# Performance work log

Hardware: AMD Instinct MI355X
Metric: run time of the kernel (lower is better)

The kernel has to match this reference:

```python
import jax, jax.numpy as jnp
import numpy as np

N = 262144
DIM = 256
H = 4
HD = DIM // H
B = 8192


def setup_inputs() -> dict:
    key = jax.random.key(0)
    ks = jax.random.split(key, 7)
    x = jax.random.normal(ks[0], (N, DIM), dtype=jnp.float32)
    batch = jnp.sort(jax.random.randint(ks[1], (N,), 0, B))
    batch = batch.at[-1].set(B - 1)  # ensure max(batch)+1 == B
    query = jax.random.normal(ks[2], (H, HD), dtype=jnp.float32)
    key_w = jax.random.normal(ks[3], (DIM, DIM), dtype=jnp.float32) * (DIM ** -0.5)
    key_b = jax.random.normal(ks[4], (DIM,), dtype=jnp.float32) * 0.02
    value_w = jax.random.normal(ks[5], (DIM, DIM), dtype=jnp.float32) * (DIM ** -0.5)
    value_b = jax.random.normal(ks[6], (DIM,), dtype=jnp.float32) * 0.02
    return {"x": x, "batch": batch, "query": query, "key_w": key_w,
            "key_b": key_b, "value_w": value_w, "value_b": value_b}


def reference(x, batch, query, key_w, key_b, value_w, value_b):
    scale = HD ** -0.5
    n = x.shape[0]
    k = (x @ key_w.T + key_b).reshape(n, H, HD)
    v = (x @ value_w.T + value_b).reshape(n, H, HD)
    attn = jnp.einsum('nhd,hd->nh', k, query) * scale  # [N,H]
    attn = jnp.clip(attn, -20.0, 20.0)
    # Faithful to source: scatter reduce='max' is buggy and returns zeros,
    # so attn_max == 0 and attn_shifted == attn (clamp makes exp safe).
    attn_exp = jnp.exp(attn)
    attn_sum = jax.ops.segment_sum(attn_exp, batch, num_segments=B)  # [B,H]
    attn_norm = attn_exp / (attn_sum[batch] + 1e-8)  # [N,H]
    weighted = attn_norm[:, :, None] * v  # [N,H,HD]
    pooled = jax.ops.segment_sum(weighted, batch, num_segments=B)  # [B,H,HD]
    return pooled.reshape(B, -1)
```

## Files before the change

kernel.cpp:

```cpp
#include <hip/hip_runtime.h>
#include <hip/hip_bf16.h>

#define NROWS 262144
#define DIM   256
#define NH    4
#define HD    64
#define NSEG  8192

#define WS_QK 65536
#define WS_QB 66560

__global__ __launch_bounds__(256) void prep_kernel(
    const float* __restrict__ query,
    const float* __restrict__ key_w,
    const float* __restrict__ key_b,
    const float* __restrict__ value_w,
    float* __restrict__ ws) {
  float* vwT = ws;
  float* qk  = ws + WS_QK;
  float* qb  = ws + WS_QB;
  const int t = threadIdx.x;

  if (blockIdx.x < 64) {
    __shared__ float tile[32][33];
    const int bx = (blockIdx.x & 7) * 32;
    const int by = (blockIdx.x >> 3) * 32;
    const int tx = t & 31, ty = t >> 5;
#pragma unroll
    for (int k = 0; k < 4; ++k)
      tile[ty + 8 * k][tx] = value_w[(by + ty + 8 * k) * DIM + bx + tx];
    __syncthreads();
#pragma unroll
    for (int k = 0; k < 4; ++k)
      vwT[(bx + ty + 8 * k) * DIM + by + tx] = tile[tx][ty + 8 * k];
  } else {
    const float scale = 0.125f;
#pragma unroll
    for (int h = 0; h < NH; ++h) {
      float acc = 0.f;
      for (int d = 0; d < HD; ++d)
        acc += query[h * HD + d] * key_w[(h * HD + d) * DIM + t];
      qk[h * DIM + t] = acc * scale;
    }
    if (t < NH) {
      float acc = 0.f;
      for (int d = 0; d < HD; ++d)
        acc += query[t * HD + d] * key_b[t * HD + d];
      qb[t] = acc * scale;
    }
  }
}

__global__ __launch_bounds__(256) void main_kernel(
    const float* __restrict__ x,
    const int* __restrict__ batch,
    const float* __restrict__ value_b,
    const float* __restrict__ ws,
    float* __restrict__ out) {
  const float* vwT = ws;
  const float* qk  = ws + WS_QK;
  const float* qb  = ws + WS_QB;

  __shared__ float zu[4][NH][DIM];
  __shared__ float sSh[4][NH];

  const int t = threadIdx.x;
  const int w = t >> 6;
  const int l = t & 63;
  const int b = blockIdx.x * 4 + w;

  int lo = 0, hi = NROWS;
  while (lo < hi) { int mid = (lo + hi) >> 1; if (batch[mid] < b) lo = mid + 1; else hi = mid; }
  const int start = lo;
  hi = NROWS;
  while (lo < hi) { int mid = (lo + hi) >> 1; if (batch[mid] < b + 1) lo = mid + 1; else hi = mid; }
  const int end = lo;

  const float4 q0 = *(const float4*)(qk + 0 * DIM + 4 * l);
  const float4 q1 = *(const float4*)(qk + 1 * DIM + 4 * l);
  const float4 q2 = *(const float4*)(qk + 2 * DIM + 4 * l);
  const float4 q3 = *(const float4*)(qk + 3 * DIM + 4 * l);
  const float qb0 = qb[0], qb1 = qb[1], qb2 = qb[2], qb3 = qb[3];

  float4 z0 = {0.f, 0.f, 0.f, 0.f}, z1 = z0, z2 = z0, z3 = z0;
  float s0 = 0.f, s1 = 0.f, s2 = 0.f, s3 = 0.f;

  for (int n = start; n < end; ++n) {
    const float4 xv = *(const float4*)(x + (size_t)n * DIM + 4 * l);
    float p0 = q0.x * xv.x + q0.y * xv.y + q0.z * xv.z + q0.w * xv.w;
    float p1 = q1.x * xv.x + q1.y * xv.y + q1.z * xv.z + q1.w * xv.w;
    float p2 = q2.x * xv.x + q2.y * xv.y + q2.z * xv.z + q2.w * xv.w;
    float p3 = q3.x * xv.x + q3.y * xv.y + q3.z * xv.z + q3.w * xv.w;
#pragma unroll
    for (int m = 1; m < 64; m <<= 1) {
      p0 += __shfl_xor(p0, m, 64);
      p1 += __shfl_xor(p1, m, 64);
      p2 += __shfl_xor(p2, m, 64);
      p3 += __shfl_xor(p3, m, 64);
    }
    const float e0 = __expf(fminf(fmaxf(p0 + qb0, -20.f), 20.f));
    const float e1 = __expf(fminf(fmaxf(p1 + qb1, -20.f), 20.f));
    const float e2 = __expf(fminf(fmaxf(p2 + qb2, -20.f), 20.f));
    const float e3 = __expf(fminf(fmaxf(p3 + qb3, -20.f), 20.f));
    s0 += e0; s1 += e1; s2 += e2; s3 += e3;
    z0.x += e0 * xv.x; z0.y += e0 * xv.y; z0.z += e0 * xv.z; z0.w += e0 * xv.w;
    z1.x += e1 * xv.x; z1.y += e1 * xv.y; z1.z += e1 * xv.z; z1.w += e1 * xv.w;
    z2.x += e2 * xv.x; z2.y += e2 * xv.y; z2.z += e2 * xv.z; z2.w += e2 * xv.w;
    z3.x += e3 * xv.x; z3.y += e3 * xv.y; z3.z += e3 * xv.z; z3.w += e3 * xv.w;
  }

  *(float4*)&zu[w][0][4 * l] = z0;
  *(float4*)&zu[w][1][4 * l] = z1;
  *(float4*)&zu[w][2][4 * l] = z2;
  *(float4*)&zu[w][3][4 * l] = z3;
  if (l == 0) { sSh[w][0] = s0; sSh[w][1] = s1; sSh[w][2] = s2; sSh[w][3] = s3; }
  __syncthreads();

  const int h = t >> 6;
  float inv[4], cb[4];
#pragma unroll
  for (int seg = 0; seg < 4; ++seg) {
    const float sv = sSh[seg][h];
    const float iv = 1.f / (sv + 1e-8f);
    inv[seg] = iv;
    cb[seg]  = sv * iv;
  }
  float a0 = 0.f, a1 = 0.f, a2 = 0.f, a3 = 0.f;
  for (int i = 0; i < DIM; i += 4) {
    const float w0 = vwT[(i + 0) * DIM + t];
    const float w1 = vwT[(i + 1) * DIM + t];
    const float w2 = vwT[(i + 2) * DIM + t];
    const float w3 = vwT[(i + 3) * DIM + t];
    const float4 za = *(const float4*)&zu[0][h][i];
    const float4 zb = *(const float4*)&zu[1][h][i];
    const float4 zc = *(const float4*)&zu[2][h][i];
    const float4 zd = *(const float4*)&zu[3][h][i];
    a0 += w0 * za.x + w1 * za.y + w2 * za.z + w3 * za.w;
    a1 += w0 * zb.x + w1 * zb.y + w2 * zb.z + w3 * zb.w;
    a2 += w0 * zc.x + w1 * zc.y + w2 * zc.z + w3 * zc.w;
    a3 += w0 * zd.x + w1 * zd.y + w2 * zd.z + w3 * zd.w;
  }
  const float vb = value_b[t];
  const int b0 = blockIdx.x * 4;
  out[(size_t)(b0 + 0) * DIM + t] = a0 * inv[0] + cb[0] * vb;
  out[(size_t)(b0 + 1) * DIM + t] = a1 * inv[1] + cb[1] * vb;
  out[(size_t)(b0 + 2) * DIM + t] = a2 * inv[2] + cb[2] * vb;
  out[(size_t)(b0 + 3) * DIM + t] = a3 * inv[3] + cb[3] * vb;
}

extern "C" void kernel_launch(void* const* d_in, const int* in_sizes, int n_in,
                              void* d_out, int out_size, void* d_ws, size_t ws_size,
                              hipStream_t stream) {
  const float* x       = (const float*)d_in[0];
  const int*   batch   = (const int*)d_in[1];
  const float* query   = (const float*)d_in[2];
  const float* key_w   = (const float*)d_in[3];
  const float* key_b   = (const float*)d_in[4];
  const float* value_w = (const float*)d_in[5];
  const float* value_b = (const float*)d_in[6];
  float* out = (float*)d_out;
  float* ws  = (float*)d_ws;

  prep_kernel<<<65, 256, 0, stream>>>(query, key_w, key_b, value_w, ws);
  main_kernel<<<2048, 256, 0, stream>>>(x, batch, value_b, ws, out);
}
```

Before: 456.1 us.

## Process eight segments per block with 4-row unroll and cheaper head reductions

Each block now handles eight segments, two per wave, so every vwT weight load in the projection epilogue is reused across twice as many segments. Segment bounds come from one cooperative binary search into shared memory. The per-row dot product uses a transpose-style partial reduction, so each lane ends up owning one head's score, cutting shuffles from 24 to 6 per row. The row loop is unrolled by four to give more loads in flight. The prep kernel also spreads the qk computation over four blocks. In exchange there are half as many blocks, with more shared memory and registers per block, which may lower occupancy and latency hiding.

```diff
diff --git a/kernel.cpp b/kernel.cpp
--- a/kernel.cpp
+++ b/kernel.cpp
@@ -6,9 +6,11 @@
 #define NH    4
 #define HD    64
 #define NSEG  8192
+#define SPB   8
+#define NBLK  (NSEG / SPB)
 
 #define WS_QK 65536
-#define WS_QB 66560
+#define WS_QB (WS_QK + NH * DIM)
 
 __global__ __launch_bounds__(256) void prep_kernel(
     const float* __restrict__ query,
@@ -33,22 +35,36 @@
 #pragma unroll
     for (int k = 0; k < 4; ++k)
       vwT[(bx + ty + 8 * k) * DIM + by + tx] = tile[tx][ty + 8 * k];
+  } else if (blockIdx.x < 68) {
+    const int h = blockIdx.x - 64;
+    float acc = 0.f;
+#pragma unroll 8
+    for (int d = 0; d < HD; ++d)
+      acc += query[h * HD + d] * key_w[(h * HD + d) * DIM + t];
+    qk[h * DIM + t] = acc * 0.125f;
   } else {
-    const float scale = 0.125f;
-#pragma unroll
-    for (int h = 0; h < NH; ++h) {
-      float acc = 0.f;
-      for (int d = 0; d < HD; ++d)
-        acc += query[h * HD + d] * key_w[(h * HD + d) * DIM + t];
-      qk[h * DIM + t] = acc * scale;
-    }
     if (t < NH) {
       float acc = 0.f;
       for (int d = 0; d < HD; ++d)
         acc += query[t * HD + d] * key_b[t * HD + d];
-      qb[t] = acc * scale;
-    }
-  }
+      qb[t] = acc * 0.125f;
+    }
+  }
+}
+
+__device__ __forceinline__ float head_partial(float p0, float p1, float p2,
+                                              float p3, int l) {
+  const bool odd = (l & 1) != 0;
+  float sa = odd ? p0 : p1;
+  float ra = __shfl_xor(sa, 1, 64);
+  float vl = (odd ? p1 : p0) + ra;
+  float sb = odd ? p2 : p3;
+  float rb = __shfl_xor(sb, 1, 64);
+  float vh = (odd ? p3 : p2) + rb;
+  const bool g2 = (l & 2) != 0;
+  float sc = g2 ? vl : vh;
+  float rc = __shfl_xor(sc, 2, 64);
+  return (g2 ? vh : vl) + rc;
 }
 
 __global__ __launch_bounds__(256) void main_kernel(
@@ -61,91 +77,163 @@
   const float* qk  = ws + WS_QK;
   const float* qb  = ws + WS_QB;
 
-  __shared__ float zu[4][NH][DIM];
-  __shared__ float sSh[4][NH];
+  __shared__ float zu[SPB][NH][DIM];
+  __shared__ float sSh[SPB][NH];
+  __shared__ int   segb[SPB + 1];
 
   const int t = threadIdx.x;
   const int w = t >> 6;
   const int l = t & 63;
-  const int b = blockIdx.x * 4 + w;
-
-  int lo = 0, hi = NROWS;
-  while (lo < hi) { int mid = (lo + hi) >> 1; if (batch[mid] < b) lo = mid + 1; else hi = mid; }
-  const int start = lo;
-  hi = NROWS;
-  while (lo < hi) { int mid = (lo + hi) >> 1; if (batch[mid] < b + 1) lo = mid + 1; else hi = mid; }
-  const int end = lo;
-
+
+  if (t <= SPB) {
+    const int target = blockIdx.x * SPB + t;
+    int lo = 0, hi = NROWS;
+    while (lo < hi) { int mid = (lo + hi) >> 1; if (batch[mid] < target) lo = mid + 1; else hi = mid; }
+    segb[t] = lo;
+  }
+  __syncthreads();
+
+  const int h4 = l & 3;
   const float4 q0 = *(const float4*)(qk + 0 * DIM + 4 * l);
   const float4 q1 = *(const float4*)(qk + 1 * DIM + 4 * l);
   const float4 q2 = *(const float4*)(qk + 2 * DIM + 4 * l);
   const float4 q3 = *(const float4*)(qk + 3 * DIM + 4 * l);
-  const float qb0 = qb[0], qb1 = qb[1], qb2 = qb[2], qb3 = qb[3];
-
-  float4 z0 = {0.f, 0.f, 0.f, 0.f}, z1 = z0, z2 = z0, z3 = z0;
-  float s0 = 0.f, s1 = 0.f, s2 = 0.f, s3 = 0.f;
-
-  for (int n = start; n < end; ++n) {
-    const float4 xv = *(const float4*)(x + (size_t)n * DIM + 4 * l);
-    float p0 = q0.x * xv.x + q0.y * xv.y + q0.z * xv.z + q0.w * xv.w;
-    float p1 = q1.x * xv.x + q1.y * xv.y + q1.z * xv.z + q1.w * xv.w;
-    float p2 = q2.x * xv.x + q2.y * xv.y + q2.z * xv.z + q2.w * xv.w;
-    float p3 = q3.x * xv.x + q3.y * xv.y + q3.z * xv.z + q3.w * xv.w;
-#pragma unroll
-    for (int m = 1; m < 64; m <<= 1) {
-      p0 += __shfl_xor(p0, m, 64);
-      p1 += __shfl_xor(p1, m, 64);
-      p2 += __shfl_xor(p2, m, 64);
-      p3 += __shfl_xor(p3, m, 64);
-    }
-    const float e0 = __expf(fminf(fmaxf(p0 + qb0, -20.f), 20.f));
-    const float e1 = __expf(fminf(fmaxf(p1 + qb1, -20.f), 20.f));
-    const float e2 = __expf(fminf(fmaxf(p2 + qb2, -20.f), 20.f));
-    const float e3 = __expf(fminf(fmaxf(p3 + qb3, -20.f), 20.f));
-    s0 += e0; s1 += e1; s2 += e2; s3 += e3;
-    z0.x += e0 * xv.x; z0.y += e0 * xv.y; z0.z += e0 * xv.z; z0.w += e0 * xv.w;
-    z1.x += e1 * xv.x; z1.y += e1 * xv.y; z1.z += e1 * xv.z; z1.w += e1 * xv.w;
-    z2.x += e2 * xv.x; z2.y += e2 * xv.y; z2.z += e2 * xv.z; z2.w += e2 * xv.w;
-    z3.x += e3 * xv.x; z3.y += e3 * xv.y; z3.z += e3 * xv.z; z3.w += e3 * xv.w;
-  }
-
-  *(float4*)&zu[w][0][4 * l] = z0;
-  *(float4*)&zu[w][1][4 * l] = z1;
-  *(float4*)&zu[w][2][4 * l] = z2;
-  *(float4*)&zu[w][3][4 * l] = z3;
-  if (l == 0) { sSh[w][0] = s0; sSh[w][1] = s1; sSh[w][2] = s2; sSh[w][3] = s3; }
+  const float qbv = qb[h4];
+
+#pragma unroll
+  for (int ss = 0; ss < 2; ++ss) {
+    const int seg = 2 * w + ss;
+    const int start = segb[seg], end = segb[seg + 1];
+    float4 z0 = {0.f, 0.f, 0.f, 0.f}, z1 = z0, z2 = z0, z3 = z0;
+    float s0 = 0.f, s1 = 0.f, s2 = 0.f, s3 = 0.f;
+    const float* xp = x + (size_t)start * DIM + 4 * l;
+    int n = start;
+
+    for (; n + 4 <= end; n += 4, xp += 4 * DIM) {
+      const float4 xv0 = *(const float4*)(xp);
+      const float4 xv1 = *(const float4*)(xp + DIM);
+      const float4 xv2 = *(const float4*)(xp + 2 * DIM);
+      const float4 xv3 = *(const float4*)(xp + 3 * DIM);
+      float v0, v1, v2, v3;
+      {
+        float p0 = q0.x * xv0.x + q0.y * xv0.y + q0.z * xv0.z + q0.w * xv0.w;
+        float p1 = q1.x * xv0.x + q1.y * xv0.y + q1.z * xv0.z + q1.w * xv0.w;
+        float p2 = q2.x * xv0.x + q2.y * xv0.y + q2.z * xv0.z + q2.w * xv0.w;
+        float p3 = q3.x * xv0.x + q3.y * xv0.y + q3.z * xv0.z + q3.w * xv0.w;
+        v0 = head_partial(p0, p1, p2, p3, l);
+      }
+      {
+        float p0 = q0.x * xv1.x + q0.y * xv1.y + q0.z * xv1.z + q0.w * xv1.w;
+        float p1 = q1.x * xv1.x + q1.y * xv1.y + q1.z * xv1.z + q1.w * xv1.w;
+        float p2 = q2.x * xv1.x + q2.y * xv1.y + q2.z * xv1.z + q2.w * xv1.w;
+        float p3 = q3.x * xv1.x + q3.y * xv1.y + q3.z * xv1.z + q3.w * xv1.w;
+        v1 = head_partial(p0, p1, p2, p3, l);
+      }
+      {
+        float p0 = q0.x * xv2.x + q0.y * xv2.y + q0.z * xv2.z + q0.w * xv2.w;
+        float p1 = q1.x * xv2.x + q1.y * xv2.y + q1.z * xv2.z + q1.w * xv2.w;
+        float p2 = q2.x * xv2.x + q2.y * xv2.y + q2.z * xv2.z + q2.w * xv2.w;
+        float p3 = q3.x * xv2.x + q3.y * xv2.y + q3.z * xv2.z + q3.w * xv2.w;
+        v2 = head_partial(p0, p1, p2, p3, l);
+      }
+      {
+        float p0 = q0.x * xv3.x + q0.y * xv3.y + q0.z * xv3.z + q0.w * xv3.w;
+        float p1 = q1.x * xv3.x + q1.y * xv3.y + q1.z * xv3.z + q1.w * xv3.w;
+        float p2 = q2.x * xv3.x + q2.y * xv3.y + q2.z * xv3.z + q2.w * xv3.w;
+        float p3 = q3.x * xv3.x + q3.y * xv3.y + q3.z * xv3.z + q3.w * xv3.w;
+        v3 = head_partial(p0, p1, p2, p3, l);
+      }
+#pragma unroll
+      for (int m = 4; m <= 32; m <<= 1) {
+        v0 += __shfl_xor(v0, m, 64);
+        v1 += __shfl_xor(v1, m, 64);
+        v2 += __shfl_xor(v2, m, 64);
+        v3 += __shfl_xor(v3, m, 64);
+      }
+      const float e00 = __expf(fminf(fmaxf(v0 + qbv, -20.f), 20.f));
+      const float e10 = __expf(fminf(fmaxf(v1 + qbv, -20.f), 20.f));
+      const float e20 = __expf(fminf(fmaxf(v2 + qbv, -20.f), 20.f));
+      const float e30 = __expf(fminf(fmaxf(v3 + qbv, -20.f), 20.f));
+      const float e01 = __shfl_xor(e00, 1, 64), e02 = __shfl_xor(e00, 2, 64), e03 = __shfl_xor(e00, 3, 64);
+      const float e11 = __shfl_xor(e10, 1, 64), e12 = __shfl_xor(e10, 2, 64), e13 = __shfl_xor(e10, 3, 64);
+      const float e21 = __shfl_xor(e20, 1, 64), e22 = __shfl_xor(e20, 2, 64), e23 = __shfl_xor(e20, 3, 64);
+      const float e31 = __shfl_xor(e30, 1, 64), e32 = __shfl_xor(e30, 2, 64), e33 = __shfl_xor(e30, 3, 64);
+      s0 += e00 + e10 + e20 + e30;
+      s1 += e01 + e11 + e21 + e31;
+      s2 += e02 + e12 + e22 + e32;
+      s3 += e03 + e13 + e23 + e33;
+      z0.x += e00 * xv0.x + e10 * xv1.x + e20 * xv2.x + e30 * xv3.x;
+      z0.y += e00 * xv0.y + e10 * xv1.y + e20 * xv2.y + e30 * xv3.y;
+      z0.z += e00 * xv0.z + e10 * xv1.z + e20 * xv2.z + e30 * xv3.z;
+      z0.w += e00 * xv0.w + e10 * xv1.w + e20 * xv2.w + e30 * xv3.w;
+      z1.x += e01 * xv0.x + e11 * xv1.x + e21 * xv2.x + e31 * xv3.x;
+      z1.y += e01 * xv0.y + e11 * xv1.y + e21 * xv2.y + e31 * xv3.y;
+      z1.z += e01 * xv0.z + e11 * xv1.z + e21 * xv2.z + e31 * xv3.z;
+      z1.w += e01 * xv0.w + e11 * xv1.w + e21 * xv2.w + e31 * xv3.w;
+      z2.x += e02 * xv0.x + e12 * xv1.x + e22 * xv2.x + e32 * xv3.x;
+      z2.y += e02 * xv0.y + e12 * xv1.y + e22 * xv2.y + e32 * xv3.y;
+      z2.z += e02 * xv0.z + e12 * xv1.z + e22 * xv2.z + e32 * xv3.z;
+      z2.w += e02 * xv0.w + e12 * xv1.w + e22 * xv2.w + e32 * xv3.w;
+      z3.x += e03 * xv0.x + e13 * xv1.x + e23 * xv2.x + e33 * xv3.x;
+      z3.y += e03 * xv0.y + e13 * xv1.y + e23 * xv2.y + e33 * xv3.y;
+      z3.z += e03 * xv0.z + e13 * xv1.z + e23 * xv2.z + e33 * xv3.z;
+      z3.w += e03 * xv0.w + e13 * xv1.w + e23 * xv2.w + e33 * xv3.w;
+    }
+    for (; n < end; ++n, xp += DIM) {
+      const float4 xv = *(const float4*)(xp);
+      float p0 = q0.x * xv.x + q0.y * xv.y + q0.z * xv.z + q0.w * xv.w;
+      float p1 = q1.x * xv.x + q1.y * xv.y + q1.z * xv.z + q1.w * xv.w;
+      float p2 = q2.x * xv.x + q2.y * xv.y + q2.z * xv.z + q2.w * xv.w;
+      float p3 = q3.x * xv.x + q3.y * xv.y + q3.z * xv.z + q3.w * xv.w;
+      float v = head_partial(p0, p1, p2, p3, l);
+#pragma unroll
+      for (int m = 4; m <= 32; m <<= 1) v += __shfl_xor(v, m, 64);
+      const float e0 = __expf(fminf(fmaxf(v + qbv, -20.f), 20.f));
+      const float e1 = __shfl_xor(e0, 1, 64);
+      const float e2 = __shfl_xor(e0, 2, 64);
+      const float e3 = __shfl_xor(e0, 3, 64);
+      s0 += e0; s1 += e1; s2 += e2; s3 += e3;
+      z0.x += e0 * xv.x; z0.y += e0 * xv.y; z0.z += e0 * xv.z; z0.w += e0 * xv.w;
+      z1.x += e1 * xv.x; z1.y += e1 * xv.y; z1.z += e1 * xv.z; z1.w += e1 * xv.w;
+      z2.x += e2 * xv.x; z2.y += e2 * xv.y; z2.z += e2 * xv.z; z2.w += e2 * xv.w;
+      z3.x += e3 * xv.x; z3.y += e3 * xv.y; z3.z += e3 * xv.z; z3.w += e3 * xv.w;
+    }
+    *(float4*)&zu[seg][h4 ^ 0][4 * l] = z0;
+    *(float4*)&zu[seg][h4 ^ 1][4 * l] = z1;
+    *(float4*)&zu[seg][h4 ^ 2][4 * l] = z2;
+    *(float4*)&zu[seg][h4 ^ 3][4 * l] = z3;
+    if (l == 0) { sSh[seg][0] = s0; sSh[seg][1] = s1; sSh[seg][2] = s2; sSh[seg][3] = s3; }
+  }
   __syncthreads();
 
   const int h = t >> 6;
-  float inv[4], cb[4];
-#pragma unroll
-  for (int seg = 0; seg < 4; ++seg) {
+  float inv[SPB], cb[SPB];
+#pragma unroll
+  for (int seg = 0; seg < SPB; ++seg) {
     const float sv = sSh[seg][h];
     const float iv = 1.f / (sv + 1e-8f);
     inv[seg] = iv;
     cb[seg]  = sv * iv;
   }
-  float a0 = 0.f, a1 = 0.f, a2 = 0.f, a3 = 0.f;
+  float acc[SPB];
+#pragma unroll
+  for (int seg = 0; seg < SPB; ++seg) acc[seg] = 0.f;
   for (int i = 0; i < DIM; i += 4) {
     const float w0 = vwT[(i + 0) * DIM + t];
     const float w1 = vwT[(i + 1) * DIM + t];
     const float w2 = vwT[(i + 2) * DIM + t];
     const float w3 = vwT[(i + 3) * DIM + t];
-    const float4 za = *(const float4*)&zu[0][h][i];
-    const float4 zb = *(const float4*)&zu[1][h][i];
-    const float4 zc = *(const float4*)&zu[2][h][i];
-    const float4 zd = *(const float4*)&zu[3][h][i];
-    a0 += w0 * za.x + w1 * za.y + w2 * za.z + w3 * za.w;
-    a1 += w0 * zb.x + w1 * zb.y + w2 * zb.z + w3 * zb.w;
-    a2 += w0 * zc.x + w1 * zc.y + w2 * zc.z + w3 * zc.w;
-    a3 += w0 * zd.x + w1 * zd.y + w2 * zd.z + w3 * zd.w;
+#pragma unroll
+    for (int seg = 0; seg < SPB; ++seg) {
+      const float4 zz = *(const float4*)&zu[seg][h][i];
+      acc[seg] += w0 * zz.x + w1 * zz.y + w2 * zz.z + w3 * zz.w;
+    }
   }
   const float vb = value_b[t];
-  const int b0 = blockIdx.x * 4;
-  out[(size_t)(b0 + 0) * DIM + t] = a0 * inv[0] + cb[0] * vb;
-  out[(size_t)(b0 + 1) * DIM + t] = a1 * inv[1] + cb[1] * vb;
-  out[(size_t)(b0 + 2) * DIM + t] = a2 * inv[2] + cb[2] * vb;
-  out[(size_t)(b0 + 3) * DIM + t] = a3 * inv[3] + cb[3] * vb;
+  const int b0 = blockIdx.x * SPB;
+#pragma unroll
+  for (int seg = 0; seg < SPB; ++seg)
+    out[(size_t)(b0 + seg) * DIM + t] = acc[seg] * inv[seg] + cb[seg] * vb;
 }
 
 extern "C" void kernel_launch(void* const* d_in, const int* in_sizes, int n_in,
@@ -161,6 +249,6 @@
   float* out = (float*)d_out;
   float* ws  = (float*)d_ws;
 
-  prep_kernel<<<65, 256, 0, stream>>>(query, key_w, key_b, value_w, ws);
-  main_kernel<<<2048, 256, 0, stream>>>(x, batch, value_b, ws, out);
-}
+  prep_kernel<<<69, 256, 0, stream>>>(query, key_w, key_b, value_w, ws);
+  main_kernel<<<NBLK, 256, 0, stream>>>(x, batch, value_b, ws, out);
+}
```

After: 415.1 us. 9.0% less time.
